# Performance work log

Measured on AMD Instinct MI355X. Metric: run time of the kernel, lower is better.

The kernel has to match this reference:

```python
import jax, jax.numpy as jnp
import numpy as np

DIM = 2048
N_HEADS = 32
HEAD_DIM = DIM // N_HEADS
D_FF = 4 * DIM
EPS = 1e-5


def layernorm(x, g, b):
    mu = jnp.mean(x, axis=-1, keepdims=True)
    var = jnp.mean(jnp.square(x - mu), axis=-1, keepdims=True)
    return (x - mu) * jax.lax.rsqrt(var + EPS) * g + b


def setup_inputs() -> dict:
    key = jax.random.key(0)
    ks = jax.random.split(key, 12)
    s = 0.02
    # Linear weights stored as [in, out] (y = x @ W + b), equivalent math to torch's x @ W.T
    return {
        "x": jax.random.normal(ks[0], (2, 2048, DIM), jnp.float32),
        "w_qkv": jax.random.normal(ks[1], (DIM, 3 * DIM), jnp.float32) * s,
        "b_qkv": jnp.zeros((3 * DIM,), jnp.float32),
        "w_o": jax.random.normal(ks[2], (DIM, DIM), jnp.float32) * s,
        "b_o": jnp.zeros((DIM,), jnp.float32),
        "g1": jnp.ones((DIM,), jnp.float32),
        "beta1": jnp.zeros((DIM,), jnp.float32),
        "w1": jax.random.normal(ks[3], (DIM, D_FF), jnp.float32) * s,
        "b1": jnp.zeros((D_FF,), jnp.float32),
        "w2": jax.random.normal(ks[4], (D_FF, DIM), jnp.float32) * s,
        "b2": jnp.zeros((DIM,), jnp.float32),
        "g2": jnp.ones((DIM,), jnp.float32),
        "beta2": jnp.zeros((DIM,), jnp.float32),
    }


def reference(x, w_qkv, b_qkv, w_o, b_o, g1, beta1, w1, b1, w2, b2, g2, beta2):
    B, T, _ = x.shape
    residual = x
    h = layernorm(x, g1, beta1)
    qkv = h @ w_qkv + b_qkv                      # [B,T,3*DIM]
    qkv = qkv.reshape(B, T, 3, N_HEADS, HEAD_DIM)
    qkv = jnp.transpose(qkv, (2, 0, 3, 1, 4))    # [3,B,H,T,D]
    q, k, v = qkv[0], qkv[1], qkv[2]
    scores = jnp.einsum("bhtd,bhsd->bhts", q, k) / np.sqrt(HEAD_DIM).astype(np.float32)
    attn = jax.nn.softmax(scores, axis=-1)       # full T x T (non-causal), as in source
    out = jnp.einsum("bhts,bhsd->bhtd", attn, v)
    out = jnp.transpose(out, (0, 2, 1, 3)).reshape(B, T, DIM)
    h = out @ w_o + b_o
    x = h + residual
    residual = x
    h = layernorm(x, g2, beta2)
    h = jax.nn.gelu(h @ w1 + b1, approximate=False)  # torch nn.GELU default = exact erf
    h = h @ w2 + b2
    return h + residual
```

## Files before the change

kernel.cpp:

```cpp
#include <hip/hip_runtime.h>
#include <hip/hip_bf16.h>

#define DIM  2048
#define DFF  8192
#define NH   32
#define HD   64
#define TT   2048
#define MM   4096

typedef __attribute__((ext_vector_type(4))) float f32x4;
typedef __attribute__((ext_vector_type(4))) unsigned int u32x4;
typedef __attribute__((ext_vector_type(2))) unsigned int u32x2;

#define MFMA16(ACC, A, B) \
  asm volatile("v_mfma_f32_16x16x32_bf16 %0, %1, %2, %0" : "+v"(ACC) : "v"(A), "v"(B))

#define GL16(GP, LP)                                                     \
  __builtin_amdgcn_global_load_lds(                                      \
      (const __attribute__((address_space(1))) void*)(GP),               \
      (__attribute__((address_space(3))) void*)(LP), 16, 0, 0)

__device__ __forceinline__ unsigned int f2bu(float f) {
  union { __hip_bfloat16 h; unsigned short u; } c;
  c.h = __float2bfloat16(f);
  return (unsigned int)c.u;
}

__global__ __launch_bounds__(256)
void transpose_cvt(const float* __restrict__ in, __hip_bfloat16* __restrict__ out,
                   int R, int C) {
  __shared__ float tile[32][33];
  const int tx = threadIdx.x, ty = threadIdx.y;
  const int bx = blockIdx.x * 32, by = blockIdx.y * 32;
#pragma unroll
  for (int i = 0; i < 32; i += 8)
    tile[ty + i][tx] = in[(size_t)(by + ty + i) * C + bx + tx];
  __syncthreads();
#pragma unroll
  for (int i = 0; i < 32; i += 8)
    out[(size_t)(bx + ty + i) * R + by + tx] = __float2bfloat16(tile[tx][ty + i]);
}

__global__ __launch_bounds__(256)
void ln_kernel(const float* __restrict__ in, const float* __restrict__ gw,
               const float* __restrict__ bw, __hip_bfloat16* __restrict__ out) {
  const int row = blockIdx.x;
  const int t = threadIdx.x;
  const float* x = in + (size_t)row * DIM;
  const float4 v0 = ((const float4*)x)[t * 2];
  const float4 v1 = ((const float4*)x)[t * 2 + 1];
  float s  = v0.x + v0.y + v0.z + v0.w + v1.x + v1.y + v1.z + v1.w;
  float ss = v0.x*v0.x + v0.y*v0.y + v0.z*v0.z + v0.w*v0.w
           + v1.x*v1.x + v1.y*v1.y + v1.z*v1.z + v1.w*v1.w;
#pragma unroll
  for (int o = 32; o >= 1; o >>= 1) { s += __shfl_xor(s, o); ss += __shfl_xor(ss, o); }
  __shared__ float red[8];
  if ((t & 63) == 0) { red[t >> 6] = s; red[4 + (t >> 6)] = ss; }
  __syncthreads();
  s  = red[0] + red[1] + red[2] + red[3];
  ss = red[4] + red[5] + red[6] + red[7];
  const float mean = s * (1.0f / DIM);
  const float rstd = rsqrtf(ss * (1.0f / DIM) - mean * mean + 1e-5f);
  const float4 g0 = ((const float4*)gw)[t * 2], g1 = ((const float4*)gw)[t * 2 + 1];
  const float4 b0 = ((const float4*)bw)[t * 2], b1 = ((const float4*)bw)[t * 2 + 1];
  uint4 o;
  o.x = f2bu((v0.x - mean) * rstd * g0.x + b0.x) | (f2bu((v0.y - mean) * rstd * g0.y + b0.y) << 16);
  o.y = f2bu((v0.z - mean) * rstd * g0.z + b0.z) | (f2bu((v0.w - mean) * rstd * g0.w + b0.w) << 16);
  o.z = f2bu((v1.x - mean) * rstd * g1.x + b1.x) | (f2bu((v1.y - mean) * rstd * g1.y + b1.y) << 16);
  o.w = f2bu((v1.z - mean) * rstd * g1.z + b1.z) | (f2bu((v1.w - mean) * rstd * g1.w + b1.w) << 16);
  *(uint4*)((char*)out + ((size_t)row * DIM + t * 8) * 2) = o;
}

template <int EPI>
__global__ __launch_bounds__(256)
void gemm_bt(const __hip_bfloat16* __restrict__ A, const __hip_bfloat16* __restrict__ Bt,
             const float* __restrict__ bias, const float* __restrict__ res,
             void* __restrict__ o0, void* __restrict__ o1, void* __restrict__ o2,
             int M, int N, int K) {
  __shared__ __hip_bfloat16 As[128 * 32];
  __shared__ __hip_bfloat16 Bs[128 * 32];
  const int tid = threadIdx.x;
  const int l = tid & 63, w = tid >> 6;
  const int wr = w >> 1, wc = w & 1;
  const int g = l >> 4, q15 = l & 15;
  const int bm = blockIdx.y * 128, bn = blockIdx.x * 128;

  f32x4 acc[4][4];
#pragma unroll
  for (int a = 0; a < 4; ++a)
#pragma unroll
    for (int b = 0; b < 4; ++b) acc[a][b] = (f32x4)0.0f;

  const __hip_bfloat16* aSrc = A  + (size_t)(bm + (tid >> 2)) * K + (tid & 3) * 8;
  const __hip_bfloat16* bSrc = Bt + (size_t)(bn + (tid >> 2)) * K + (tid & 3) * 8;
  __hip_bfloat16* aDst = As + tid * 8;
  __hip_bfloat16* bDst = Bs + tid * 8;
  const size_t rowStep = (size_t)64 * K;

  for (int kt = 0; kt < K; kt += 32) {
    GL16(aSrc + kt,            aDst);
    GL16(aSrc + rowStep + kt,  aDst + 2048);
    GL16(bSrc + kt,            bDst);
    GL16(bSrc + rowStep + kt,  bDst + 2048);
    __syncthreads();
    u32x4 af[4], bf[4];
#pragma unroll
    for (int rb = 0; rb < 4; ++rb)
      af[rb] = *(const u32x4*)(As + (wr * 64 + rb * 16 + q15) * 32 + g * 8);
#pragma unroll
    for (int cb = 0; cb < 4; ++cb)
      bf[cb] = *(const u32x4*)(Bs + (wc * 64 + cb * 16 + q15) * 32 + g * 8);
#pragma unroll
    for (int rb = 0; rb < 4; ++rb)
#pragma unroll
      for (int cb = 0; cb < 4; ++cb) MFMA16(acc[rb][cb], af[rb], bf[cb]);
    __syncthreads();
  }

#pragma unroll
  for (int rb = 0; rb < 4; ++rb) {
    const int row0 = bm + wr * 64 + rb * 16 + g * 4;
#pragma unroll
    for (int cb = 0; cb < 4; ++cb) {
      const int col = bn + wc * 64 + cb * 16 + q15;
      const float bv = bias[col];
#pragma unroll
      for (int i = 0; i < 4; ++i) {
        const int m = row0 + i;
        float v = acc[rb][cb][i] + bv;
        if constexpr (EPI == 0) {
          const int sel = col >> 11, hd = col & 2047, h = hd >> 6, d = hd & 63;
          const int b = m >> 11, t = m & 2047;
          if (sel == 0) {
            ((__hip_bfloat16*)o0)[((size_t)(b * NH + h) * TT + t) * HD + d] =
                __float2bfloat16(v * 0.125f);
          } else if (sel == 1) {
            ((__hip_bfloat16*)o1)[((size_t)(b * NH + h) * TT + t) * HD + d] =
                __float2bfloat16(v);
          } else {
            ((__hip_bfloat16*)o2)[((size_t)(b * NH + h) * HD + d) * TT + t] =
                __float2bfloat16(v);
          }
        } else if constexpr (EPI == 1) {
          ((float*)o0)[(size_t)m * N + col] = v + res[(size_t)m * N + col];
        } else if constexpr (EPI == 2) {
          ((__hip_bfloat16*)o0)[(size_t)m * N + col] =
              __float2bfloat16(0.5f * v * (1.0f + erff(v * 0.70710678118654752f)));
        } else {
          ((float*)o0)[(size_t)m * N + col] = v + res[(size_t)m * N + col];
        }
      }
    }
  }
}

__global__ __launch_bounds__(256)
void attn_kernel(const __hip_bfloat16* __restrict__ Q, const __hip_bfloat16* __restrict__ Kx,
                 const __hip_bfloat16* __restrict__ Vt, __hip_bfloat16* __restrict__ out) {
  __shared__ unsigned int Plds[4][2048];
  const int tid = threadIdx.x;
  const int l = tid & 63, w = tid >> 6;
  const int g = l >> 4, q15 = l & 15;
  const int bh = blockIdx.x >> 3;
  const int q0 = (blockIdx.x & 7) * 256 + w * 64;
  const __hip_bfloat16* Qb = Q  + (size_t)bh * TT * HD;
  const __hip_bfloat16* Kb = Kx + (size_t)bh * TT * HD;
  const __hip_bfloat16* Vb = Vt + (size_t)bh * HD * TT;
  unsigned int* Pw = Plds[w];

  u32x4 qf[4][2];
#pragma unroll
  for (int rb = 0; rb < 4; ++rb)
#pragma unroll
    for (int ks = 0; ks < 2; ++ks)
      qf[rb][ks] = *(const u32x4*)(Qb + (size_t)(q0 + rb * 16 + q15) * HD + ks * 32 + g * 8);

  f32x4 acc[4][4];
#pragma unroll
  for (int a = 0; a < 4; ++a)
#pragma unroll
    for (int b = 0; b < 4; ++b) acc[a][b] = (f32x4)0.0f;
  float mstat[4] = {-3e38f, -3e38f, -3e38f, -3e38f};
  float lstat[4] = {0.f, 0.f, 0.f, 0.f};

  for (int s0 = 0; s0 < TT; s0 += 64) {
    f32x4 st[4][4];
#pragma unroll
    for (int a = 0; a < 4; ++a)
#pragma unroll
      for (int b = 0; b < 4; ++b) st[a][b] = (f32x4)0.0f;
#pragma unroll
    for (int ks = 0; ks < 2; ++ks) {
      u32x4 kf[4];
#pragma unroll
      for (int cb = 0; cb < 4; ++cb)
        kf[cb] = *(const u32x4*)(Kb + (size_t)(s0 + cb * 16 + q15) * HD + ks * 32 + g * 8);
#pragma unroll
      for (int cb = 0; cb < 4; ++cb)
#pragma unroll
        for (int rb = 0; rb < 4; ++rb) MFMA16(st[cb][rb], kf[cb], qf[rb][ks]);
    }
#pragma unroll
    for (int rb = 0; rb < 4; ++rb) {
      float pm = st[0][rb][0];
#pragma unroll
      for (int cb = 0; cb < 4; ++cb)
#pragma unroll
        for (int i = 0; i < 4; ++i) pm = fmaxf(pm, st[cb][rb][i]);
      pm = fmaxf(pm, __shfl_xor(pm, 16));
      pm = fmaxf(pm, __shfl_xor(pm, 32));
      const float mnew = fmaxf(mstat[rb], pm);
      const float corr = __expf(mstat[rb] - mnew);
      mstat[rb] = mnew;
      float rs = 0.f;
#pragma unroll
      for (int cb = 0; cb < 4; ++cb)
#pragma unroll
        for (int i = 0; i < 4; ++i) {
          const float p = __expf(st[cb][rb][i] - mnew);
          st[cb][rb][i] = p;
          rs += p;
        }
      rs += __shfl_xor(rs, 16);
      rs += __shfl_xor(rs, 32);
      lstat[rb] = lstat[rb] * corr + rs;
#pragma unroll
      for (int db = 0; db < 4; ++db)
#pragma unroll
        for (int i = 0; i < 4; ++i) acc[db][rb][i] *= corr;
      const int row = rb * 16 + q15;
      const int rx = row & 7;
#pragma unroll
      for (int cb = 0; cb < 4; ++cb) {
        const unsigned int lo = f2bu(st[cb][rb][0]) | (f2bu(st[cb][rb][1]) << 16);
        const unsigned int hi = f2bu(st[cb][rb][2]) | (f2bu(st[cb][rb][3]) << 16);
        const int seg = (cb * 2 + (g >> 1)) ^ rx;
        u32x2 pk = {lo, hi};
        *(u32x2*)(Pw + row * 32 + seg * 4 + (g & 1) * 2) = pk;
      }
    }
#pragma unroll
    for (int ks2 = 0; ks2 < 2; ++ks2) {
      u32x4 vf[4], pf[4];
#pragma unroll
      for (int db = 0; db < 4; ++db)
        vf[db] = *(const u32x4*)(Vb + (size_t)(db * 16 + q15) * TT + s0 + ks2 * 32 + g * 8);
#pragma unroll
      for (int rb = 0; rb < 4; ++rb) {
        const int row = rb * 16 + q15;
        const int seg = (ks2 * 4 + g) ^ (row & 7);
        pf[rb] = *(const u32x4*)(Pw + row * 32 + seg * 4);
      }
#pragma unroll
      for (int db = 0; db < 4; ++db)
#pragma unroll
        for (int rb = 0; rb < 4; ++rb) MFMA16(acc[db][rb], vf[db], pf[rb]);
    }
  }
  const int b = bh >> 5, hh = bh & 31;
#pragma unroll
  for (int rb = 0; rb < 4; ++rb) {
    const float inv = 1.0f / lstat[rb];
    const size_t trow = (size_t)(b * TT + q0 + rb * 16 + q15);
#pragma unroll
    for (int db = 0; db < 4; ++db) {
      const unsigned int lo = f2bu(acc[db][rb][0] * inv) | (f2bu(acc[db][rb][1] * inv) << 16);
      const unsigned int hi = f2bu(acc[db][rb][2] * inv) | (f2bu(acc[db][rb][3] * inv) << 16);
      u32x2 pk = {lo, hi};
      *(u32x2*)(out + trow * DIM + hh * 64 + db * 16 + g * 4) = pk;
    }
  }
}

extern "C" void kernel_launch(void* const* d_in, const int* in_sizes, int n_in,
                              void* d_out, int out_size, void* d_ws, size_t ws_size,
                              hipStream_t stream) {
  (void)in_sizes; (void)n_in; (void)out_size; (void)ws_size;
  const float* x     = (const float*)d_in[0];
  const float* w_qkv = (const float*)d_in[1];
  const float* b_qkv = (const float*)d_in[2];
  const float* w_o   = (const float*)d_in[3];
  const float* b_o   = (const float*)d_in[4];
  const float* g1    = (const float*)d_in[5];
  const float* be1   = (const float*)d_in[6];
  const float* w1    = (const float*)d_in[7];
  const float* b1    = (const float*)d_in[8];
  const float* w2    = (const float*)d_in[9];
  const float* b2    = (const float*)d_in[10];
  const float* g2    = (const float*)d_in[11];
  const float* be2   = (const float*)d_in[12];

  char* ws = (char*)d_ws;
  size_t off = 0;
  auto alloc = [&](size_t bytes) {
    void* p = ws + off;
    off += (bytes + 255) & ~(size_t)255;
    return p;
  };
  __hip_bfloat16* WqkvT = (__hip_bfloat16*)alloc((size_t)6144 * 2048 * 2);
  __hip_bfloat16* WoT   = (__hip_bfloat16*)alloc((size_t)2048 * 2048 * 2);
  __hip_bfloat16* W1T   = (__hip_bfloat16*)alloc((size_t)8192 * 2048 * 2);
  __hip_bfloat16* W2T   = (__hip_bfloat16*)alloc((size_t)2048 * 8192 * 2);
  __hip_bfloat16* hbuf  = (__hip_bfloat16*)alloc((size_t)MM * DIM * 2);
  float*          xres  = (float*)alloc((size_t)MM * DIM * 4);
  __hip_bfloat16* Qb    = (__hip_bfloat16*)alloc((size_t)MM * DIM * 2);
  __hip_bfloat16* Kb    = (__hip_bfloat16*)alloc((size_t)MM * DIM * 2);
  __hip_bfloat16* Vtb   = (__hip_bfloat16*)alloc((size_t)MM * DIM * 2);
  __hip_bfloat16* attno = (__hip_bfloat16*)alloc((size_t)MM * DIM * 2);
  __hip_bfloat16* f1    = Qb;

  const dim3 tb(32, 8);
  transpose_cvt<<<dim3(6144 / 32, 2048 / 32), tb, 0, stream>>>(w_qkv, WqkvT, 2048, 6144);
  transpose_cvt<<<dim3(2048 / 32, 2048 / 32), tb, 0, stream>>>(w_o, WoT, 2048, 2048);
  transpose_cvt<<<dim3(8192 / 32, 2048 / 32), tb, 0, stream>>>(w1, W1T, 2048, 8192);
  transpose_cvt<<<dim3(2048 / 32, 8192 / 32), tb, 0, stream>>>(w2, W2T, 8192, 2048);

  ln_kernel<<<MM, 256, 0, stream>>>(x, g1, be1, hbuf);
  gemm_bt<0><<<dim3(6144 / 128, MM / 128), 256, 0, stream>>>(
      hbuf, WqkvT, b_qkv, nullptr, Qb, Kb, Vtb, MM, 6144, 2048);
  attn_kernel<<<512, 256, 0, stream>>>(Qb, Kb, Vtb, attno);
  gemm_bt<1><<<dim3(2048 / 128, MM / 128), 256, 0, stream>>>(
      attno, WoT, b_o, x, xres, nullptr, nullptr, MM, 2048, 2048);
  ln_kernel<<<MM, 256, 0, stream>>>(xres, g2, be2, hbuf);
  gemm_bt<2><<<dim3(8192 / 128, MM / 128), 256, 0, stream>>>(
      hbuf, W1T, b1, nullptr, f1, nullptr, nullptr, MM, 8192, 2048);
  gemm_bt<3><<<dim3(2048 / 128, MM / 128), 256, 0, stream>>>(
      f1, W2T, b2, xres, d_out, nullptr, nullptr, MM, 2048, 8192);
}
```

Before: 802.1 us.

## Replace big GEMMs with 256x256 double-buffered swizzled kernel and split-K W2

```diff
diff --git a/kernel.cpp b/kernel.cpp
--- a/kernel.cpp
+++ b/kernel.cpp
@@ -11,6 +11,7 @@
 typedef __attribute__((ext_vector_type(4))) float f32x4;
 typedef __attribute__((ext_vector_type(4))) unsigned int u32x4;
 typedef __attribute__((ext_vector_type(2))) unsigned int u32x2;
+typedef unsigned short ushort_t;
 
 #define MFMA16(ACC, A, B) \
   asm volatile("v_mfma_f32_16x16x32_bf16 %0, %1, %2, %0" : "+v"(ACC) : "v"(A), "v"(B))
@@ -72,65 +73,159 @@
 }
 
 template <int EPI>
-__global__ __launch_bounds__(256)
-void gemm_bt(const __hip_bfloat16* __restrict__ A, const __hip_bfloat16* __restrict__ Bt,
+__global__ __launch_bounds__(512, 2)
+void gemm256(const __hip_bfloat16* __restrict__ Abf, const __hip_bfloat16* __restrict__ Btbf,
              const float* __restrict__ bias, const float* __restrict__ res,
              void* __restrict__ o0, void* __restrict__ o1, void* __restrict__ o2,
-             int M, int N, int K) {
-  __shared__ __hip_bfloat16 As[128 * 32];
-  __shared__ __hip_bfloat16 Bs[128 * 32];
+             int M, int N, int K, int nkt) {
+  __shared__ ushort_t lds[2][2][16384];
   const int tid = threadIdx.x;
   const int l = tid & 63, w = tid >> 6;
-  const int wr = w >> 1, wc = w & 1;
+  const int wm = w >> 2, wn = w & 3;
   const int g = l >> 4, q15 = l & 15;
-  const int bm = blockIdx.y * 128, bn = blockIdx.x * 128;
-
-  f32x4 acc[4][4];
-#pragma unroll
-  for (int a = 0; a < 4; ++a)
+
+  const int nby = M >> 8;
+  const int nwg = (N >> 8) * nby;
+  int id = blockIdx.x;
+  {
+    const int qq = nwg >> 3, rr = nwg & 7;
+    const int xcd = id & 7, pos = id >> 3;
+    id = (xcd < rr ? xcd * (qq + 1) : rr * (qq + 1) + (xcd - rr) * qq) + pos;
+  }
+  const int bm = (id % nby) << 8;
+  const int bn = (id / nby) << 8;
+  const int k0 = (EPI == 4) ? (int)blockIdx.y * (nkt << 6) : 0;
+
+  const ushort_t* Au = (const ushort_t*)Abf;
+  const ushort_t* Bu = (const ushort_t*)Btbf;
+  const int sr = tid >> 3;
+  const int sc = (((tid & 7) ^ (sr & 7)) << 3);
+  const ushort_t* aBase = Au + (size_t)(bm + sr) * K + (k0 + sc);
+  const ushort_t* bBase = Bu + (size_t)(bn + sr) * K + (k0 + sc);
+  const int dOff = (w << 9) + (l << 3);
+
+#define STG(ab, grp, dbuf, kkk)                                          \
+  GL16(((ab) ? bBase : aBase) + (size_t)((grp) << 6) * K + (kkk),        \
+       &lds[dbuf][ab][((grp) << 12) + dOff])
+
+#define AFRAG(dbuf, m, ks)                                               \
+  (*(const u32x4*)&lds[dbuf][0][((((wm) << 7) + ((m) << 4) + q15) << 6) + \
+                                (((((ks) << 2) | g) ^ (q15 & 7)) << 3)])
+#define BFRAG(dbuf, n, ks)                                               \
+  (*(const u32x4*)&lds[dbuf][1][((((wn) << 6) + ((n) << 4) + q15) << 6) + \
+                                (((((ks) << 2) | g) ^ (q15 & 7)) << 3)])
+
+  f32x4 acc[8][4];
+#pragma unroll
+  for (int a = 0; a < 8; ++a)
 #pragma unroll
     for (int b = 0; b < 4; ++b) acc[a][b] = (f32x4)0.0f;
 
-  const __hip_bfloat16* aSrc = A  + (size_t)(bm + (tid >> 2)) * K + (tid & 3) * 8;
-  const __hip_bfloat16* bSrc = Bt + (size_t)(bn + (tid >> 2)) * K + (tid & 3) * 8;
-  __hip_bfloat16* aDst = As + tid * 8;
-  __hip_bfloat16* bDst = Bs + tid * 8;
-  const size_t rowStep = (size_t)64 * K;
-
-  for (int kt = 0; kt < K; kt += 32) {
-    GL16(aSrc + kt,            aDst);
-    GL16(aSrc + rowStep + kt,  aDst + 2048);
-    GL16(bSrc + kt,            bDst);
-    GL16(bSrc + rowStep + kt,  bDst + 2048);
-    __syncthreads();
-    u32x4 af[4], bf[4];
-#pragma unroll
-    for (int rb = 0; rb < 4; ++rb)
-      af[rb] = *(const u32x4*)(As + (wr * 64 + rb * 16 + q15) * 32 + g * 8);
-#pragma unroll
-    for (int cb = 0; cb < 4; ++cb)
-      bf[cb] = *(const u32x4*)(Bs + (wc * 64 + cb * 16 + q15) * 32 + g * 8);
-#pragma unroll
-    for (int rb = 0; rb < 4; ++rb)
-#pragma unroll
-      for (int cb = 0; cb < 4; ++cb) MFMA16(acc[rb][cb], af[rb], bf[cb]);
-    __syncthreads();
-  }
-
-#pragma unroll
-  for (int rb = 0; rb < 4; ++rb) {
-    const int row0 = bm + wr * 64 + rb * 16 + g * 4;
-#pragma unroll
-    for (int cb = 0; cb < 4; ++cb) {
-      const int col = bn + wc * 64 + cb * 16 + q15;
-      const float bv = bias[col];
+  STG(1, 0, 0, 0); STG(1, 1, 0, 0); STG(1, 2, 0, 0); STG(1, 3, 0, 0);
+  STG(0, 0, 0, 0); STG(0, 2, 0, 0); STG(0, 1, 0, 0); STG(0, 3, 0, 0);
+  asm volatile("s_waitcnt vmcnt(2)" ::: "memory");
+  __builtin_amdgcn_s_barrier();
+
+  int cur = 0;
+  for (int kt = 0; kt < nkt; ++kt) {
+    const int nxt = cur ^ 1;
+    const bool hn = (kt + 1) < nkt;
+    const int kk = (kt + 1) << 6;
+    u32x4 bf[4][2], af[2][2];
+
+    if (hn) { STG(1, 0, nxt, kk); STG(1, 1, nxt, kk); }
+#pragma unroll
+    for (int n = 0; n < 4; ++n)
+#pragma unroll
+      for (int ks = 0; ks < 2; ++ks) bf[n][ks] = BFRAG(cur, n, ks);
+#pragma unroll
+    for (int mm = 0; mm < 2; ++mm)
+#pragma unroll
+      for (int ks = 0; ks < 2; ++ks) af[mm][ks] = AFRAG(cur, mm, ks);
+    __builtin_amdgcn_s_barrier();
+    asm volatile("s_waitcnt lgkmcnt(0)" ::: "memory");
+    __builtin_amdgcn_s_setprio(1);
+#pragma unroll
+    for (int ks = 0; ks < 2; ++ks)
+#pragma unroll
+      for (int mm = 0; mm < 2; ++mm)
+#pragma unroll
+        for (int n = 0; n < 4; ++n) MFMA16(acc[mm][n], af[mm][ks], bf[n][ks]);
+    __builtin_amdgcn_s_setprio(0);
+    __builtin_amdgcn_s_barrier();
+
+    if (hn) { STG(1, 2, nxt, kk); STG(1, 3, nxt, kk); }
+#pragma unroll
+    for (int mm = 0; mm < 2; ++mm)
+#pragma unroll
+      for (int ks = 0; ks < 2; ++ks) af[mm][ks] = AFRAG(cur, 2 + mm, ks);
+    if (hn) asm volatile("s_waitcnt vmcnt(4)" ::: "memory");
+    else    asm volatile("s_waitcnt vmcnt(0)" ::: "memory");
+    __builtin_amdgcn_s_barrier();
+    asm volatile("s_waitcnt lgkmcnt(0)" ::: "memory");
+    __builtin_amdgcn_s_setprio(1);
+#pragma unroll
+    for (int ks = 0; ks < 2; ++ks)
+#pragma unroll
+      for (int mm = 0; mm < 2; ++mm)
+#pragma unroll
+        for (int n = 0; n < 4; ++n) MFMA16(acc[2 + mm][n], af[mm][ks], bf[n][ks]);
+    __builtin_amdgcn_s_setprio(0);
+    __builtin_amdgcn_s_barrier();
+
+    if (hn) { STG(0, 0, nxt, kk); STG(0, 2, nxt, kk); }
+#pragma unroll
+    for (int mm = 0; mm < 2; ++mm)
+#pragma unroll
+      for (int ks = 0; ks < 2; ++ks) af[mm][ks] = AFRAG(cur, 4 + mm, ks);
+    __builtin_amdgcn_s_barrier();
+    asm volatile("s_waitcnt lgkmcnt(0)" ::: "memory");
+    __builtin_amdgcn_s_setprio(1);
+#pragma unroll
+    for (int ks = 0; ks < 2; ++ks)
+#pragma unroll
+      for (int mm = 0; mm < 2; ++mm)
+#pragma unroll
+        for (int n = 0; n < 4; ++n) MFMA16(acc[4 + mm][n], af[mm][ks], bf[n][ks]);
+    __builtin_amdgcn_s_setprio(0);
+    __builtin_amdgcn_s_barrier();
+
+    if (hn) { STG(0, 1, nxt, kk); STG(0, 3, nxt, kk); }
+#pragma unroll
+    for (int mm = 0; mm < 2; ++mm)
+#pragma unroll
+      for (int ks = 0; ks < 2; ++ks) af[mm][ks] = AFRAG(cur, 6 + mm, ks);
+    if (hn) asm volatile("s_waitcnt vmcnt(2)" ::: "memory");
+    __builtin_amdgcn_s_barrier();
+    asm volatile("s_waitcnt lgkmcnt(0)" ::: "memory");
+    __builtin_amdgcn_s_setprio(1);
+#pragma unroll
+    for (int ks = 0; ks < 2; ++ks)
+#pragma unroll
+      for (int mm = 0; mm < 2; ++mm)
+#pragma unroll
+        for (int n = 0; n < 4; ++n) MFMA16(acc[6 + mm][n], af[mm][ks], bf[n][ks]);
+    __builtin_amdgcn_s_setprio(0);
+    __builtin_amdgcn_s_barrier();
+
+    cur = nxt;
+  }
+
+#pragma unroll
+  for (int m = 0; m < 8; ++m) {
+    const int row0 = bm + (wm << 7) + (m << 4) + (g << 2);
+#pragma unroll
+    for (int n = 0; n < 4; ++n) {
+      const int col = bn + (wn << 6) + (n << 4) + q15;
+      float bv = 0.0f;
+      if constexpr (EPI != 4) bv = bias[col];
 #pragma unroll
       for (int i = 0; i < 4; ++i) {
-        const int m = row0 + i;
-        float v = acc[rb][cb][i] + bv;
+        const int mrow = row0 + i;
+        float v = acc[m][n][i] + bv;
         if constexpr (EPI == 0) {
           const int sel = col >> 11, hd = col & 2047, h = hd >> 6, d = hd & 63;
-          const int b = m >> 11, t = m & 2047;
+          const int b = mrow >> 11, t = mrow & 2047;
           if (sel == 0) {
             ((__hip_bfloat16*)o0)[((size_t)(b * NH + h) * TT + t) * HD + d] =
                 __float2bfloat16(v * 0.125f);
@@ -141,14 +236,94 @@
             ((__hip_bfloat16*)o2)[((size_t)(b * NH + h) * HD + d) * TT + t] =
                 __float2bfloat16(v);
           }
-        } else if constexpr (EPI == 1) {
-          ((float*)o0)[(size_t)m * N + col] = v + res[(size_t)m * N + col];
         } else if constexpr (EPI == 2) {
-          ((__hip_bfloat16*)o0)[(size_t)m * N + col] =
+          ((__hip_bfloat16*)o0)[(size_t)mrow * N + col] =
               __float2bfloat16(0.5f * v * (1.0f + erff(v * 0.70710678118654752f)));
         } else {
-          ((float*)o0)[(size_t)m * N + col] = v + res[(size_t)m * N + col];
+          ((float*)(blockIdx.y ? o1 : o0))[(size_t)mrow * N + col] = v;
         }
+      }
+    }
+  }
+#undef STG
+#undef AFRAG
+#undef BFRAG
+}
+
+__global__ __launch_bounds__(256)
+void combine2(const float* __restrict__ p0, const float* __restrict__ p1,
+              const float* __restrict__ bias, const float* __restrict__ res,
+              float* __restrict__ out) {
+  const size_t i = ((size_t)blockIdx.x * 256 + threadIdx.x) << 2;
+  const float4 a = *(const float4*)(p0 + i);
+  const float4 b = *(const float4*)(p1 + i);
+  const float4 r = *(const float4*)(res + i);
+  const float4 bi = *(const float4*)(bias + (i & (DIM - 1)));
+  float4 o;
+  o.x = a.x + b.x + r.x + bi.x;
+  o.y = a.y + b.y + r.y + bi.y;
+  o.z = a.z + b.z + r.z + bi.z;
+  o.w = a.w + b.w + r.w + bi.w;
+  *(float4*)(out + i) = o;
+}
+
+template <int EPI>
+__global__ __launch_bounds__(256)
+void gemm_bt(const __hip_bfloat16* __restrict__ A, const __hip_bfloat16* __restrict__ Bt,
+             const float* __restrict__ bias, const float* __restrict__ res,
+             void* __restrict__ o0, int M, int N, int K) {
+  __shared__ __hip_bfloat16 As[128 * 32];
+  __shared__ __hip_bfloat16 Bs[128 * 32];
+  const int tid = threadIdx.x;
+  const int l = tid & 63, w = tid >> 6;
+  const int wr = w >> 1, wc = w & 1;
+  const int g = l >> 4, q15 = l & 15;
+  const int bm = blockIdx.y * 128, bn = blockIdx.x * 128;
+
+  f32x4 acc[4][4];
+#pragma unroll
+  for (int a = 0; a < 4; ++a)
+#pragma unroll
+    for (int b = 0; b < 4; ++b) acc[a][b] = (f32x4)0.0f;
+
+  const __hip_bfloat16* aSrc = A  + (size_t)(bm + (tid >> 2)) * K + (tid & 3) * 8;
+  const __hip_bfloat16* bSrc = Bt + (size_t)(bn + (tid >> 2)) * K + (tid & 3) * 8;
+  __hip_bfloat16* aDst = As + tid * 8;
+  __hip_bfloat16* bDst = Bs + tid * 8;
+  const size_t rowStep = (size_t)64 * K;
+
+  for (int kt = 0; kt < K; kt += 32) {
+    GL16(aSrc + kt,            aDst);
+    GL16(aSrc + rowStep + kt,  aDst + 2048);
+    GL16(bSrc + kt,            bDst);
+    GL16(bSrc + rowStep + kt,  bDst + 2048);
+    __syncthreads();
+    u32x4 af[4], bf[4];
+#pragma unroll
+    for (int rb = 0; rb < 4; ++rb)
+      af[rb] = *(const u32x4*)(As + (wr * 64 + rb * 16 + q15) * 32 + g * 8);
+#pragma unroll
+    for (int cb = 0; cb < 4; ++cb)
+      bf[cb] = *(const u32x4*)(Bs + (wc * 64 + cb * 16 + q15) * 32 + g * 8);
+#pragma unroll
+    for (int rb = 0; rb < 4; ++rb)
+#pragma unroll
+      for (int cb = 0; cb < 4; ++cb) MFMA16(acc[rb][cb], af[rb], bf[cb]);
+    __syncthreads();
+  }
+
+#pragma unroll
+  for (int rb = 0; rb < 4; ++rb) {
+    const int row0 = bm + wr * 64 + rb * 16 + g * 4;
+#pragma unroll
+    for (int cb = 0; cb < 4; ++cb) {
+      const int col = bn + wc * 64 + cb * 16 + q15;
+      const float bv = bias[col];
+#pragma unroll
+      for (int i = 0; i < 4; ++i) {
+        const int m = row0 + i;
+        float v = acc[rb][cb][i] + bv;
+        ((float*)o0)[(size_t)m * N + col] = v + res[(size_t)m * N + col];
       }
     }
   }
@@ -308,6 +483,8 @@
   __hip_bfloat16* Vtb   = (__hip_bfloat16*)alloc((size_t)MM * DIM * 2);
   __hip_bfloat16* attno = (__hip_bfloat16*)alloc((size_t)MM * DIM * 2);
   __hip_bfloat16* f1    = Qb;
+  float* p0 = (float*)ws;
+  float* p1 = (float*)(ws + (size_t)MM * DIM * 4);
 
   const dim3 tb(32, 8);
   transpose_cvt<<<dim3(6144 / 32, 2048 / 32), tb, 0, stream>>>(w_qkv, WqkvT, 2048, 6144);
@@ -316,14 +493,15 @@
   transpose_cvt<<<dim3(2048 / 32, 8192 / 32), tb, 0, stream>>>(w2, W2T, 8192, 2048);
 
   ln_kernel<<<MM, 256, 0, stream>>>(x, g1, be1, hbuf);
-  gemm_bt<0><<<dim3(6144 / 128, MM / 128), 256, 0, stream>>>(
-      hbuf, WqkvT, b_qkv, nullptr, Qb, Kb, Vtb, MM, 6144, 2048);
+  gemm256<0><<<dim3((6144 / 256) * (MM / 256)), 512, 0, stream>>>(
+      hbuf, WqkvT, b_qkv, nullptr, Qb, Kb, Vtb, MM, 6144, 2048, 32);
   attn_kernel<<<512, 256, 0, stream>>>(Qb, Kb, Vtb, attno);
   gemm_bt<1><<<dim3(2048 / 128, MM / 128), 256, 0, stream>>>(
-      attno, WoT, b_o, x, xres, nullptr, nullptr, MM, 2048, 2048);
+      attno, WoT, b_o, x, xres, MM, 2048, 2048);
   ln_kernel<<<MM, 256, 0, stream>>>(xres, g2, be2, hbuf);
-  gemm_bt<2><<<dim3(8192 / 128, MM / 128), 256, 0, stream>>>(
-      hbuf, W1T, b1, nullptr, f1, nullptr, nullptr, MM, 8192, 2048);
-  gemm_bt<3><<<dim3(2048 / 128, MM / 128), 256, 0, stream>>>(
-      f1, W2T, b2, xres, d_out, nullptr, nullptr, MM, 2048, 8192);
-}
+  gemm256<2><<<dim3((8192 / 256) * (MM / 256)), 512, 0, stream>>>(
+      hbuf, W1T, b1, nullptr, f1, nullptr, nullptr, MM, 8192, 2048, 32);
+  gemm256<4><<<dim3((2048 / 256) * (MM / 256), 2), 512, 0, stream>>>(
+      f1, W2T, nullptr, nullptr, p0, p1, nullptr, MM, 2048, 8192, 64);
+  combine2<<<(MM * DIM) / 1024, 256, 0, stream>>>(p0, p1, b2, xres, (float*)d_out);
+}
```

New measurement: 766.3 us. 4.5% less time.
